# Kernel tuning notes

Hardware: AMD Instinct MI355X
Metric: run time of the kernel (lower is better)

## Reference

```python
import jax, jax.numpy as jnp
import numpy as np

N_NODES = 10000
N_EDGES = 320000
D_IN = 256
D_OUT = 256


def setup_inputs() -> dict:
    key = jax.random.key(0)
    k1, k2, k3, k4, k5, k6 = jax.random.split(key, 6)
    feat = jax.random.normal(k1, (N_NODES, D_IN), dtype=jnp.float32)
    eweight = jax.random.uniform(k2, (N_EDGES, 1), dtype=jnp.float32)
    # Linear(in_dim*2 -> out_dim): weight [out, 2*in], bias [out]
    W = jax.random.normal(k3, (D_OUT, 2 * D_IN), dtype=jnp.float32) / np.sqrt(2 * D_IN)
    b = jax.random.normal(k4, (D_OUT,), dtype=jnp.float32) * 0.01
    src = jax.random.randint(k5, (N_EDGES,), 0, N_NODES, dtype=jnp.int64)
    dst = jax.random.randint(k6, (N_EDGES,), 0, N_NODES, dtype=jnp.int64)
    return {"feat": feat, "eweight": eweight, "W": W, "b": b, "src": src, "dst": dst}


def reference(feat, eweight, W, b, src, dst):
    n = feat.shape[0]
    # message: u_mul_e -> h[src] * ew   (broadcast [E,1] over [E,D])
    msg = feat[src] * eweight
    # mean reduce by destination: sum(msg) / in-degree
    agg = jax.ops.segment_sum(msg, dst, num_segments=n)
    deg = jax.ops.segment_sum(jnp.ones((src.shape[0],), dtype=feat.dtype), dst, num_segments=n)
    h_neigh = agg / jnp.maximum(deg, 1.0)[:, None]
    # concat aggregated with self features, then linear
    h = jnp.concatenate([h_neigh, feat], axis=-1)  # [N, 2*D]
    return h @ W.T + b
```

## Files before the change

kernel.cpp:

```cpp
#include <hip/hip_runtime.h>
#include <hip/hip_bf16.h>

#define N_NODES 10000
#define N_EDGES 320000
#define D 256
#define K_TOT 512
#define CAP 128

typedef __attribute__((ext_vector_type(8))) short bf16x8;
typedef __attribute__((ext_vector_type(4))) float f32x4;

__device__ __forceinline__ float bf2f(unsigned short u) {
  return __uint_as_float(((unsigned int)u) << 16);
}
__device__ __forceinline__ unsigned short f2bf(float f) {
  unsigned int x = __float_as_uint(f);
  unsigned int r = (x + 0x7fffu + ((x >> 16) & 1u)) >> 16;
  return (unsigned short)r;
}

#define FEAT_VECS (N_NODES * D / 8)
#define W_VECS    (D * K_TOT / 8)
#define CUR_VECS  (N_NODES / 4)
__global__ __launch_bounds__(256) void tobf16_kernel(
    const float* __restrict__ feat, const float* __restrict__ W,
    unsigned short* __restrict__ hcat, unsigned short* __restrict__ Wb,
    int* __restrict__ cursor) {
  int gid = blockIdx.x * 256 + threadIdx.x;
  const float* srcp;
  unsigned short* dstp;
  if (gid < FEAT_VECS) {
    int row = gid >> 5;
    int v = gid & 31;
    srcp = feat + (size_t)row * D + v * 8;
    dstp = hcat + (size_t)row * K_TOT + D + v * 8;
  } else if (gid < FEAT_VECS + W_VECS) {
    int g = gid - FEAT_VECS;
    int row = g >> 6;
    int v = g & 63;
    srcp = W + (size_t)row * K_TOT + v * 8;
    dstp = Wb + (size_t)row * K_TOT + v * 8;
  } else if (gid < FEAT_VECS + W_VECS + CUR_VECS) {
    int g = gid - (FEAT_VECS + W_VECS);
    reinterpret_cast<int4*>(cursor)[g] = make_int4(0, 0, 0, 0);
    return;
  } else {
    return;
  }
  float4 a = reinterpret_cast<const float4*>(srcp)[0];
  float4 b = reinterpret_cast<const float4*>(srcp)[1];
  reinterpret_cast<ushort4*>(dstp)[0] =
      make_ushort4(f2bf(a.x), f2bf(a.y), f2bf(a.z), f2bf(a.w));
  reinterpret_cast<ushort4*>(dstp)[1] =
      make_ushort4(f2bf(b.x), f2bf(b.y), f2bf(b.z), f2bf(b.w));
}

__global__ __launch_bounds__(256) void append_kernel(const int* __restrict__ src,
                                                     const int* __restrict__ dst,
                                                     const float* __restrict__ ew,
                                                     int* __restrict__ cursor,
                                                     int2* __restrict__ bucket) {
  int i = (blockIdx.x * 256 + threadIdx.x) * 2;
  if (i + 1 < N_EDGES) {
    int2 s2 = *reinterpret_cast<const int2*>(src + i);
    int2 d2 = *reinterpret_cast<const int2*>(dst + i);
    float2 w2 = *reinterpret_cast<const float2*>(ew + i);
    int pos0 = atomicAdd(&cursor[d2.x], 1);
    if (pos0 < CAP)
      bucket[(size_t)d2.x * CAP + pos0] = make_int2(s2.x, __float_as_int(w2.x));
    int pos1 = atomicAdd(&cursor[d2.y], 1);
    if (pos1 < CAP)
      bucket[(size_t)d2.y * CAP + pos1] = make_int2(s2.y, __float_as_int(w2.y));
  } else if (i < N_EDGES) {
    int d = dst[i];
    int pos = atomicAdd(&cursor[d], 1);
    if (pos < CAP)
      bucket[(size_t)d * CAP + pos] = make_int2(src[i], __float_as_int(ew[i]));
  }
}

__global__ __launch_bounds__(256) void agg_kernel(const int* __restrict__ cursor,
                                                  const int2* __restrict__ bucket,
                                                  unsigned short* __restrict__ hcat) {
  int node = (blockIdx.x * 256 + threadIdx.x) >> 6;
  int lane = threadIdx.x & 63;
  if (node >= N_NODES) return;
  int cnt = cursor[node];
  int end = min(cnt, CAP);
  const int2* bk = bucket + (size_t)node * CAP;
  float acc0 = 0.f, acc1 = 0.f, acc2 = 0.f, acc3 = 0.f;
  int i = 0;
  for (; i + 8 <= end; i += 8) {
    int4 e01 = *reinterpret_cast<const int4*>(bk + i);
    int4 e23 = *reinterpret_cast<const int4*>(bk + i + 2);
    int4 e45 = *reinterpret_cast<const int4*>(bk + i + 4);
    int4 e67 = *reinterpret_cast<const int4*>(bk + i + 6);
    ushort4 v0 = *reinterpret_cast<const ushort4*>(hcat + (size_t)e01.x * K_TOT + D + lane * 4);
    ushort4 v1 = *reinterpret_cast<const ushort4*>(hcat + (size_t)e01.z * K_TOT + D + lane * 4);
    ushort4 v2 = *reinterpret_cast<const ushort4*>(hcat + (size_t)e23.x * K_TOT + D + lane * 4);
    ushort4 v3 = *reinterpret_cast<const ushort4*>(hcat + (size_t)e23.z * K_TOT + D + lane * 4);
    ushort4 v4 = *reinterpret_cast<const ushort4*>(hcat + (size_t)e45.x * K_TOT + D + lane * 4);
    ushort4 v5 = *reinterpret_cast<const ushort4*>(hcat + (size_t)e45.z * K_TOT + D + lane * 4);
    ushort4 v6 = *reinterpret_cast<const ushort4*>(hcat + (size_t)e67.x * K_TOT + D + lane * 4);
    ushort4 v7 = *reinterpret_cast<const ushort4*>(hcat + (size_t)e67.z * K_TOT + D + lane * 4);
    float w0 = __int_as_float(e01.y), w1 = __int_as_float(e01.w);
    float w2 = __int_as_float(e23.y), w3 = __int_as_float(e23.w);
    float w4 = __int_as_float(e45.y), w5 = __int_as_float(e45.w);
    float w6 = __int_as_float(e67.y), w7 = __int_as_float(e67.w);
    acc0 += bf2f(v0.x) * w0; acc1 += bf2f(v0.y) * w0; acc2 += bf2f(v0.z) * w0; acc3 += bf2f(v0.w) * w0;
    acc0 += bf2f(v1.x) * w1; acc1 += bf2f(v1.y) * w1; acc2 += bf2f(v1.z) * w1; acc3 += bf2f(v1.w) * w1;
    acc0 += bf2f(v2.x) * w2; acc1 += bf2f(v2.y) * w2; acc2 += bf2f(v2.z) * w2; acc3 += bf2f(v2.w) * w2;
    acc0 += bf2f(v3.x) * w3; acc1 += bf2f(v3.y) * w3; acc2 += bf2f(v3.z) * w3; acc3 += bf2f(v3.w) * w3;
    acc0 += bf2f(v4.x) * w4; acc1 += bf2f(v4.y) * w4; acc2 += bf2f(v4.z) * w4; acc3 += bf2f(v4.w) * w4;
    acc0 += bf2f(v5.x) * w5; acc1 += bf2f(v5.y) * w5; acc2 += bf2f(v5.z) * w5; acc3 += bf2f(v5.w) * w5;
    acc0 += bf2f(v6.x) * w6; acc1 += bf2f(v6.y) * w6; acc2 += bf2f(v6.z) * w6; acc3 += bf2f(v6.w) * w6;
    acc0 += bf2f(v7.x) * w7; acc1 += bf2f(v7.y) * w7; acc2 += bf2f(v7.z) * w7; acc3 += bf2f(v7.w) * w7;
  }
  for (; i < end; ++i) {
    int2 sw = bk[i];
    ushort4 v = *reinterpret_cast<const ushort4*>(hcat + (size_t)sw.x * K_TOT + D + lane * 4);
    float w = __int_as_float(sw.y);
    acc0 += bf2f(v.x) * w; acc1 += bf2f(v.y) * w; acc2 += bf2f(v.z) * w; acc3 += bf2f(v.w) * w;
  }
  float inv = 1.0f / fmaxf((float)cnt, 1.0f);
  ushort4 o = make_ushort4(f2bf(acc0 * inv), f2bf(acc1 * inv),
                           f2bf(acc2 * inv), f2bf(acc3 * inv));
  *reinterpret_cast<ushort4*>(hcat + (size_t)node * K_TOT + lane * 4) = o;
}

#define GBM 64
#define GBN 64
#define GBK 64
#define LPAD 72

__global__ __launch_bounds__(256) void gemm_kernel(
    const unsigned short* __restrict__ hcat, const unsigned short* __restrict__ Wb,
    const float* __restrict__ bias, float* __restrict__ out) {
  __shared__ unsigned short As[GBM][LPAD];
  __shared__ unsigned short Bs[GBN][LPAD];

  int row0 = blockIdx.x * GBM;
  int col0 = blockIdx.y * GBN;
  int t = threadIdx.x;
  int lane = t & 63;
  int w = t >> 6;
  int wr = w >> 1;
  int wc = w & 1;
  int lhi = lane >> 4;
  int llo = lane & 15;

  f32x4 acc[2][2];
  #pragma unroll
  for (int m = 0; m < 2; ++m)
    #pragma unroll
    for (int n = 0; n < 2; ++n) acc[m][n] = (f32x4){0.f, 0.f, 0.f, 0.f};

  for (int k0 = 0; k0 < K_TOT; k0 += GBK) {
    #pragma unroll
    for (int it = 0; it < 2; ++it) {
      int idx = t + it * 256;
      int r = idx >> 3;
      int kv = (idx & 7) * 8;
      int row = row0 + r;
      uint4 v = make_uint4(0, 0, 0, 0);
      if (row < N_NODES)
        v = *reinterpret_cast<const uint4*>(hcat + (size_t)row * K_TOT + k0 + kv);
      *reinterpret_cast<uint4*>(&As[r][kv]) = v;
    }
    #pragma unroll
    for (int it = 0; it < 2; ++it) {
      int idx = t + it * 256;
      int c = idx >> 3;
      int kv = (idx & 7) * 8;
      uint4 v = *reinterpret_cast<const uint4*>(Wb + (size_t)(col0 + c) * K_TOT + k0 + kv);
      *reinterpret_cast<uint4*>(&Bs[c][kv]) = v;
    }
    __syncthreads();

    #pragma unroll
    for (int ks = 0; ks < 2; ++ks) {
      int ak = ks * 32 + lhi * 8;
      bf16x8 a[2], b[2];
      #pragma unroll
      for (int m = 0; m < 2; ++m)
        a[m] = *reinterpret_cast<const bf16x8*>(&As[wr * 32 + m * 16 + llo][ak]);
      #pragma unroll
      for (int n = 0; n < 2; ++n)
        b[n] = *reinterpret_cast<const bf16x8*>(&Bs[wc * 32 + n * 16 + llo][ak]);
      #pragma unroll
      for (int m = 0; m < 2; ++m)
        #pragma unroll
        for (int n = 0; n < 2; ++n)
          acc[m][n] = __builtin_amdgcn_mfma_f32_16x16x32_bf16(a[m], b[n], acc[m][n], 0, 0, 0);
    }
    __syncthreads();
  }

  #pragma unroll
  for (int m = 0; m < 2; ++m) {
    #pragma unroll
    for (int n = 0; n < 2; ++n) {
      int col = col0 + wc * 32 + n * 16 + llo;
      float bv = bias[col];
      #pragma unroll
      for (int r = 0; r < 4; ++r) {
        int orow = row0 + wr * 32 + m * 16 + lhi * 4 + r;
        if (orow < N_NODES)
          out[(size_t)orow * D + col] = acc[m][n][r] + bv;
      }
    }
  }
}

extern "C" void kernel_launch(void* const* d_in, const int* in_sizes, int n_in,
                              void* d_out, int out_size, void* d_ws, size_t ws_size,
                              hipStream_t stream) {
  const float* feat = (const float*)d_in[0];
  const float* ew   = (const float*)d_in[1];
  const float* W    = (const float*)d_in[2];
  const float* bias = (const float*)d_in[3];
  const int*   src  = (const int*)d_in[4];
  const int*   dst  = (const int*)d_in[5];
  float* out = (float*)d_out;

  char* ws = (char*)d_ws;
  unsigned short* hcat = (unsigned short*)ws;  ws += (size_t)N_NODES * K_TOT * sizeof(unsigned short);
  unsigned short* Wb   = (unsigned short*)ws;  ws += (size_t)D * K_TOT * sizeof(unsigned short);
  int* cursor   = (int*)ws;                    ws += N_NODES * sizeof(int);
  int2* bucket  = (int2*)ws;                   ws += (size_t)N_NODES * CAP * sizeof(int2);

  tobf16_kernel<<<(FEAT_VECS + W_VECS + CUR_VECS + 255) / 256, 256, 0, stream>>>(
      feat, W, hcat, Wb, cursor);
  append_kernel<<<(N_EDGES / 2 + 255) / 256, 256, 0, stream>>>(src, dst, ew, cursor, bucket);
  agg_kernel<<<(N_NODES * 64 + 255) / 256, 256, 0, stream>>>(cursor, bucket, hcat);

  dim3 grid((N_NODES + GBM - 1) / GBM, D / GBN);
  gemm_kernel<<<grid, 256, 0, stream>>>(hcat, Wb, bias, out);
}
```

Baseline: 72.36 us.

## Widen agg loads to 16 bytes with two nodes per wave; GEMM covers all columns

```diff
diff --git a/kernel.cpp b/kernel.cpp
--- a/kernel.cpp
+++ b/kernel.cpp
@@ -8,6 +8,7 @@
 #define CAP 128
 
 typedef __attribute__((ext_vector_type(8))) short bf16x8;
+typedef __attribute__((ext_vector_type(8))) unsigned short u16x8;
 typedef __attribute__((ext_vector_type(4))) float f32x4;
 
 __device__ __forceinline__ float bf2f(unsigned short u) {
@@ -82,54 +83,60 @@
 __global__ __launch_bounds__(256) void agg_kernel(const int* __restrict__ cursor,
                                                   const int2* __restrict__ bucket,
                                                   unsigned short* __restrict__ hcat) {
-  int node = (blockIdx.x * 256 + threadIdx.x) >> 6;
+  int wid = (blockIdx.x * 256 + threadIdx.x) >> 6;
   int lane = threadIdx.x & 63;
+  int node = wid * 2 + (lane >> 5);
+  int hl = lane & 31;
   if (node >= N_NODES) return;
   int cnt = cursor[node];
   int end = min(cnt, CAP);
   const int2* bk = bucket + (size_t)node * CAP;
-  float acc0 = 0.f, acc1 = 0.f, acc2 = 0.f, acc3 = 0.f;
+  const unsigned short* fbase = hcat + D + (size_t)hl * 8;
+  float a0 = 0.f, a1 = 0.f, a2 = 0.f, a3 = 0.f;
+  float a4 = 0.f, a5 = 0.f, a6 = 0.f, a7 = 0.f;
   int i = 0;
   for (; i + 8 <= end; i += 8) {
     int4 e01 = *reinterpret_cast<const int4*>(bk + i);
     int4 e23 = *reinterpret_cast<const int4*>(bk + i + 2);
     int4 e45 = *reinterpret_cast<const int4*>(bk + i + 4);
     int4 e67 = *reinterpret_cast<const int4*>(bk + i + 6);
-    ushort4 v0 = *reinterpret_cast<const ushort4*>(hcat + (size_t)e01.x * K_TOT + D + lane * 4);
-    ushort4 v1 = *reinterpret_cast<const ushort4*>(hcat + (size_t)e01.z * K_TOT + D + lane * 4);
-    ushort4 v2 = *reinterpret_cast<const ushort4*>(hcat + (size_t)e23.x * K_TOT + D + lane * 4);
-    ushort4 v3 = *reinterpret_cast<const ushort4*>(hcat + (size_t)e23.z * K_TOT + D + lane * 4);
-    ushort4 v4 = *reinterpret_cast<const ushort4*>(hcat + (size_t)e45.x * K_TOT + D + lane * 4);
-    ushort4 v5 = *reinterpret_cast<const ushort4*>(hcat + (size_t)e45.z * K_TOT + D + lane * 4);
-    ushort4 v6 = *reinterpret_cast<const ushort4*>(hcat + (size_t)e67.x * K_TOT + D + lane * 4);
-    ushort4 v7 = *reinterpret_cast<const ushort4*>(hcat + (size_t)e67.z * K_TOT + D + lane * 4);
+    u16x8 v0 = *reinterpret_cast<const u16x8*>(fbase + (size_t)e01.x * K_TOT);
+    u16x8 v1 = *reinterpret_cast<const u16x8*>(fbase + (size_t)e01.z * K_TOT);
+    u16x8 v2 = *reinterpret_cast<const u16x8*>(fbase + (size_t)e23.x * K_TOT);
+    u16x8 v3 = *reinterpret_cast<const u16x8*>(fbase + (size_t)e23.z * K_TOT);
+    u16x8 v4 = *reinterpret_cast<const u16x8*>(fbase + (size_t)e45.x * K_TOT);
+    u16x8 v5 = *reinterpret_cast<const u16x8*>(fbase + (size_t)e45.z * K_TOT);
+    u16x8 v6 = *reinterpret_cast<const u16x8*>(fbase + (size_t)e67.x * K_TOT);
+    u16x8 v7 = *reinterpret_cast<const u16x8*>(fbase + (size_t)e67.z * K_TOT);
     float w0 = __int_as_float(e01.y), w1 = __int_as_float(e01.w);
     float w2 = __int_as_float(e23.y), w3 = __int_as_float(e23.w);
     float w4 = __int_as_float(e45.y), w5 = __int_as_float(e45.w);
     float w6 = __int_as_float(e67.y), w7 = __int_as_float(e67.w);
-    acc0 += bf2f(v0.x) * w0; acc1 += bf2f(v0.y) * w0; acc2 += bf2f(v0.z) * w0; acc3 += bf2f(v0.w) * w0;
-    acc0 += bf2f(v1.x) * w1; acc1 += bf2f(v1.y) * w1; acc2 += bf2f(v1.z) * w1; acc3 += bf2f(v1.w) * w1;
-    acc0 += bf2f(v2.x) * w2; acc1 += bf2f(v2.y) * w2; acc2 += bf2f(v2.z) * w2; acc3 += bf2f(v2.w) * w2;
-    acc0 += bf2f(v3.x) * w3; acc1 += bf2f(v3.y) * w3; acc2 += bf2f(v3.z) * w3; acc3 += bf2f(v3.w) * w3;
-    acc0 += bf2f(v4.x) * w4; acc1 += bf2f(v4.y) * w4; acc2 += bf2f(v4.z) * w4; acc3 += bf2f(v4.w) * w4;
-    acc0 += bf2f(v5.x) * w5; acc1 += bf2f(v5.y) * w5; acc2 += bf2f(v5.z) * w5; acc3 += bf2f(v5.w) * w5;
-    acc0 += bf2f(v6.x) * w6; acc1 += bf2f(v6.y) * w6; acc2 += bf2f(v6.z) * w6; acc3 += bf2f(v6.w) * w6;
-    acc0 += bf2f(v7.x) * w7; acc1 += bf2f(v7.y) * w7; acc2 += bf2f(v7.z) * w7; acc3 += bf2f(v7.w) * w7;
+#define ACC8(v, w)                                                        \
+    a0 += bf2f((v)[0]) * (w); a1 += bf2f((v)[1]) * (w);                   \
+    a2 += bf2f((v)[2]) * (w); a3 += bf2f((v)[3]) * (w);                   \
+    a4 += bf2f((v)[4]) * (w); a5 += bf2f((v)[5]) * (w);                   \
+    a6 += bf2f((v)[6]) * (w); a7 += bf2f((v)[7]) * (w);
+    ACC8(v0, w0) ACC8(v1, w1) ACC8(v2, w2) ACC8(v3, w3)
+    ACC8(v4, w4) ACC8(v5, w5) ACC8(v6, w6) ACC8(v7, w7)
   }
   for (; i < end; ++i) {
     int2 sw = bk[i];
-    ushort4 v = *reinterpret_cast<const ushort4*>(hcat + (size_t)sw.x * K_TOT + D + lane * 4);
+    u16x8 v = *reinterpret_cast<const u16x8*>(fbase + (size_t)sw.x * K_TOT);
     float w = __int_as_float(sw.y);
-    acc0 += bf2f(v.x) * w; acc1 += bf2f(v.y) * w; acc2 += bf2f(v.z) * w; acc3 += bf2f(v.w) * w;
-  }
+    ACC8(v, w)
+  }
+#undef ACC8
   float inv = 1.0f / fmaxf((float)cnt, 1.0f);
-  ushort4 o = make_ushort4(f2bf(acc0 * inv), f2bf(acc1 * inv),
-                           f2bf(acc2 * inv), f2bf(acc3 * inv));
-  *reinterpret_cast<ushort4*>(hcat + (size_t)node * K_TOT + lane * 4) = o;
+  u16x8 o;
+  o[0] = f2bf(a0 * inv); o[1] = f2bf(a1 * inv);
+  o[2] = f2bf(a2 * inv); o[3] = f2bf(a3 * inv);
+  o[4] = f2bf(a4 * inv); o[5] = f2bf(a5 * inv);
+  o[6] = f2bf(a6 * inv); o[7] = f2bf(a7 * inv);
+  *reinterpret_cast<u16x8*>(hcat + (size_t)node * K_TOT + hl * 8) = o;
 }
 
 #define GBM 64
-#define GBN 64
 #define GBK 64
 #define LPAD 72
 
@@ -137,10 +144,9 @@
     const unsigned short* __restrict__ hcat, const unsigned short* __restrict__ Wb,
     const float* __restrict__ bias, float* __restrict__ out) {
   __shared__ unsigned short As[GBM][LPAD];
-  __shared__ unsigned short Bs[GBN][LPAD];
+  __shared__ unsigned short Bs[64][LPAD];
 
   int row0 = blockIdx.x * GBM;
-  int col0 = blockIdx.y * GBN;
   int t = threadIdx.x;
   int lane = t & 63;
   int w = t >> 6;
@@ -149,11 +155,13 @@
   int lhi = lane >> 4;
   int llo = lane & 15;
 
-  f32x4 acc[2][2];
+  f32x4 acc[4][2][2];
   #pragma unroll
-  for (int m = 0; m < 2; ++m)
-    #pragma unroll
-    for (int n = 0; n < 2; ++n) acc[m][n] = (f32x4){0.f, 0.f, 0.f, 0.f};
+  for (int c = 0; c < 4; ++c)
+    #pragma unroll
+    for (int m = 0; m < 2; ++m)
+      #pragma unroll
+      for (int n = 0; n < 2; ++n) acc[c][m][n] = (f32x4){0.f, 0.f, 0.f, 0.f};
 
   for (int k0 = 0; k0 < K_TOT; k0 += GBK) {
     #pragma unroll
@@ -167,46 +175,56 @@
         v = *reinterpret_cast<const uint4*>(hcat + (size_t)row * K_TOT + k0 + kv);
       *reinterpret_cast<uint4*>(&As[r][kv]) = v;
     }
-    #pragma unroll
-    for (int it = 0; it < 2; ++it) {
-      int idx = t + it * 256;
-      int c = idx >> 3;
-      int kv = (idx & 7) * 8;
-      uint4 v = *reinterpret_cast<const uint4*>(Wb + (size_t)(col0 + c) * K_TOT + k0 + kv);
-      *reinterpret_cast<uint4*>(&Bs[c][kv]) = v;
+
+    #pragma unroll
+    for (int c = 0; c < 4; ++c) {
+      if (c) __syncthreads();
+      #pragma unroll
+      for (int it = 0; it < 2; ++it) {
+        int idx = t + it * 256;
+        int cc = idx >> 3;
+        int kv = (idx & 7) * 8;
+        uint4 v = *reinterpret_cast<const uint4*>(
+            Wb + (size_t)(c * 64 + cc) * K_TOT + k0 + kv);
+        *reinterpret_cast<uint4*>(&Bs[cc][kv]) = v;
+      }
+      __syncthreads();
+
+      #pragma unroll
+      for (int ks = 0; ks < 2; ++ks) {
+        int ak = ks * 32 + lhi * 8;
+        bf16x8 a[2], b[2];
+        #pragma unroll
+        for (int m = 0; m < 2; ++m)
+          a[m] = *reinterpret_cast<const bf16x8*>(&As[wr * 32 + m * 16 + llo][ak]);
+        #pragma unroll
+        for (int n = 0; n < 2; ++n)
+          b[n] = *reinterpret_cast<const bf16x8*>(&Bs[wc * 32 + n * 16 + llo][ak]);
+        #pragma unroll
+        for (int m = 0; m < 2; ++m)
+          #pragma unroll
+          for (int n = 0; n < 2; ++n)
+            acc[c][m][n] =
+                __builtin_amdgcn_mfma_f32_16x16x32_bf16(a[m], b[n], acc[c][m][n], 0, 0, 0);
+      }
     }
     __syncthreads();
-
-    #pragma unroll
-    for (int ks = 0; ks < 2; ++ks) {
-      int ak = ks * 32 + lhi * 8;
-      bf16x8 a[2], b[2];
-      #pragma unroll
-      for (int m = 0; m < 2; ++m)
-        a[m] = *reinterpret_cast<const bf16x8*>(&As[wr * 32 + m * 16 + llo][ak]);
-      #pragma unroll
-      for (int n = 0; n < 2; ++n)
-        b[n] = *reinterpret_cast<const bf16x8*>(&Bs[wc * 32 + n * 16 + llo][ak]);
-      #pragma unroll
-      for (int m = 0; m < 2; ++m)
-        #pragma unroll
-        for (int n = 0; n < 2; ++n)
-          acc[m][n] = __builtin_amdgcn_mfma_f32_16x16x32_bf16(a[m], b[n], acc[m][n], 0, 0, 0);
-    }
-    __syncthreads();
   }
 
   #pragma unroll
-  for (int m = 0; m < 2; ++m) {
-    #pragma unroll
-    for (int n = 0; n < 2; ++n) {
-      int col = col0 + wc * 32 + n * 16 + llo;
-      float bv = bias[col];
-      #pragma unroll
-      for (int r = 0; r < 4; ++r) {
-        int orow = row0 + wr * 32 + m * 16 + lhi * 4 + r;
-        if (orow < N_NODES)
-          out[(size_t)orow * D + col] = acc[m][n][r] + bv;
+  for (int c = 0; c < 4; ++c) {
+    #pragma unroll
+    for (int m = 0; m < 2; ++m) {
+      #pragma unroll
+      for (int n = 0; n < 2; ++n) {
+        int col = c * 64 + wc * 32 + n * 16 + llo;
+        float bv = bias[col];
+        #pragma unroll
+        for (int r = 0; r < 4; ++r) {
+          int orow = row0 + wr * 32 + m * 16 + lhi * 4 + r;
+          if (orow < N_NODES)
+            out[(size_t)orow * D + col] = acc[c][m][n][r] + bv;
+        }
       }
     }
   }
@@ -232,8 +250,7 @@
   tobf16_kernel<<<(FEAT_VECS + W_VECS + CUR_VECS + 255) / 256, 256, 0, stream>>>(
       feat, W, hcat, Wb, cursor);
   append_kernel<<<(N_EDGES / 2 + 255) / 256, 256, 0, stream>>>(src, dst, ew, cursor, bucket);
-  agg_kernel<<<(N_NODES * 64 + 255) / 256, 256, 0, stream>>>(cursor, bucket, hcat);
-
-  dim3 grid((N_NODES + GBM - 1) / GBM, D / GBN);
-  gemm_kernel<<<grid, 256, 0, stream>>>(hcat, Wb, bias, out);
-}
+  agg_kernel<<<(N_NODES / 2 * 64 + 255) / 256, 256, 0, stream>>>(cursor, bucket, hcat);
+
+  gemm_kernel<<<dim3((N_NODES + GBM - 1) / GBM), 256, 0, stream>>>(hcat, Wb, bias, out);
+}
```

New measurement: 81.13 us. +12.1%, slower.
